# Optimization experiments

Hardware: AMD Instinct MI355X
Metric: run time of the kernel (lower is better)

## Reference

```python
import jax, jax.numpy as jnp
import numpy as np

B, TK, H = 32, 1024, 512
N = 2 * H          # hidden_dim * 2
AD = 512           # attention_dimension


def setup_inputs() -> dict:
    key = jax.random.key(0)
    ks = jax.random.split(key, 11)
    s = 0.02  # weight scale
    return {
        's_t_hat': jax.random.normal(ks[0], (B, N), jnp.float32),
        'encoder_outputs': jax.random.normal(ks[1], (B, TK, N), jnp.float32),
        'encoder_feature': jax.random.normal(ks[2], (B * TK, N), jnp.float32),
        'enc_padding_mask': jax.random.uniform(ks[3], (B, TK), jnp.float32),
        'coverage': jax.random.uniform(ks[4], (B, TK), jnp.float32),
        'r_i': jax.random.normal(ks[5], (B, TK, AD), jnp.float32),
        'W_s_w': jax.random.normal(ks[6], (N, N), jnp.float32) * s,
        'W_s_b': jax.random.normal(ks[7], (N,), jnp.float32) * s,
        'W_c_w': jax.random.normal(ks[8], (N, 1), jnp.float32) * s,
        'v_w': jax.random.normal(ks[9], (1, N), jnp.float32) * s,
        'W_r_w': jax.random.normal(ks[10], (N, AD), jnp.float32) * s,
    }


def reference(s_t_hat, encoder_outputs, encoder_feature, enc_padding_mask,
              coverage, r_i, W_s_w, W_s_b, W_c_w, v_w, W_r_w):
    b, t_k, n = encoder_outputs.shape
    # decoder feature: W_s(s_t_hat), broadcast over time
    dec_fea = s_t_hat @ W_s_w.T + W_s_b                       # [b, n]
    enc_feat = encoder_feature.reshape(b, t_k, n)             # [b, t_k, n]
    # coverage feature: W_c applied to scalar coverage per position
    cov_feat = coverage[..., None] * W_c_w[:, 0]              # [b, t_k, n]
    e = jnp.tanh(enc_feat + dec_fea[:, None, :] + cov_feat)   # [b, t_k, n]
    scores = jnp.einsum('btn,n->bt', e, v_w[0])               # [b, t_k]
    attn_ = jax.nn.softmax(scores, axis=1) * enc_padding_mask
    attn = attn_ / attn_.sum(1, keepdims=True)                # renormalized
    c_t = jnp.einsum('bt,btn->bn', attn, encoder_outputs)     # [b, n]
    coverage_new = coverage + attn                            # [b, t_k]
    # structural (LSA) branch
    Wrri = jnp.einsum('bta,na->btn', r_i, W_r_w)              # [b, t_k, n]
    e_s = jnp.tanh(Wrri + dec_fea[:, None, :])
    s2 = jnp.einsum('btn,n->bt', e_s, v_w[0])
    a_struct = (jax.nn.softmax(s2, axis=1) * enc_padding_mask)[:, None, :]  # [b,1,t_k]
    c_t_struct = jnp.einsum('bt,btn->bn', a_struct[:, 0], encoder_outputs)  # [b, n]
    return (c_t, attn, coverage_new, c_t_struct, a_struct)
```

## Files before the change

### kernel.cpp

```cpp
#include <hip/hip_runtime.h>
#include <hip/hip_bf16.h>

static constexpr int BB   = 32;
static constexpr int TKK  = 1024;
static constexpr int ND   = 1024;
static constexpr int ADIM = 512;

typedef __attribute__((ext_vector_type(8))) short bf16x8;
typedef __attribute__((ext_vector_type(4))) float f32x4;

__device__ __forceinline__ float fast_tanh(float x) {
  x = fminf(fmaxf(x, -15.f), 15.f);
  float e = __expf(2.f * x);
  return __fdividef(e - 1.f, e + 1.f);
}

__device__ __forceinline__ short f2bf(float x) {
  unsigned u = __float_as_uint(x);
  u += 0x7FFF + ((u >> 16) & 1);
  return (short)(u >> 16);
}

__device__ __forceinline__ void gload_lds16(const void* g, void* l) {
  __builtin_amdgcn_global_load_lds(
      (const __attribute__((address_space(1))) unsigned int*)g,
      (__attribute__((address_space(3))) unsigned int*)l, 16, 0, 0);
}

__global__ __launch_bounds__(256) void k_cvt2(const float* __restrict__ r_i,
    const float* __restrict__ Wr, short* __restrict__ rb, short* __restrict__ wb) {
  size_t bid = blockIdx.x;
  const float* src;
  short* dst;
  size_t i;
  if (bid < 8192) { src = r_i; dst = rb; i = bid * 256 + threadIdx.x; }
  else            { src = Wr;  dst = wb; i = (bid - 8192) * 256 + threadIdx.x; }
  float4 a = ((const float4*)src)[2 * i];
  float4 b = ((const float4*)src)[2 * i + 1];
  bf16x8 h;
  h[0] = f2bf(a.x); h[1] = f2bf(a.y); h[2] = f2bf(a.z); h[3] = f2bf(a.w);
  h[4] = f2bf(b.x); h[5] = f2bf(b.y); h[6] = f2bf(b.z); h[7] = f2bf(b.w);
  ((bf16x8*)dst)[i] = h;
}

__global__ __launch_bounds__(256) void k_decfea(const float* __restrict__ s_t_hat,
    const float* __restrict__ Wsw, const float* __restrict__ Wsb,
    float* __restrict__ dec) {
  int b  = blockIdx.x >> 3;
  int n0 = (blockIdx.x & 7) << 7;
  int w = threadIdx.x >> 6, lane = threadIdx.x & 63;
  const float4* s4 = (const float4*)(s_t_hat + (size_t)b * ND);
  float4 sv0 = s4[lane], sv1 = s4[lane + 64], sv2 = s4[lane + 128], sv3 = s4[lane + 192];
  for (int nn = 0; nn < 32; nn++) {
    int n = n0 + w * 32 + nn;
    const float4* w4 = (const float4*)(Wsw + (size_t)n * ND);
    float4 wa = w4[lane], wb = w4[lane + 64], wc = w4[lane + 128], wd = w4[lane + 192];
    float acc = sv0.x*wa.x + sv0.y*wa.y + sv0.z*wa.z + sv0.w*wa.w
              + sv1.x*wb.x + sv1.y*wb.y + sv1.z*wb.z + sv1.w*wb.w
              + sv2.x*wc.x + sv2.y*wc.y + sv2.z*wc.z + sv2.w*wc.w
              + sv3.x*wd.x + sv3.y*wd.y + sv3.z*wd.z + sv3.w*wd.w;
    #pragma unroll
    for (int off = 32; off; off >>= 1) acc += __shfl_down(acc, off);
    if (lane == 0) dec[b * ND + n] = acc + Wsb[n];
  }
}

__global__ __launch_bounds__(256) void k_scoresA(const float* __restrict__ ef,
    const float* __restrict__ dec, const float* __restrict__ Wc,
    const float* __restrict__ vw, const float* __restrict__ cov,
    float* __restrict__ scores) {
  __shared__ float sb[4];
  int bt = blockIdx.x;
  int b  = bt >> 10;
  int tid = threadIdx.x;
  float4 e = *(const float4*)(ef + (size_t)bt * ND + tid * 4);
  float4 d = *(const float4*)(dec + (size_t)b * ND + tid * 4);
  float4 w = *(const float4*)(Wc + tid * 4);
  float4 v = *(const float4*)(vw + tid * 4);
  float c = cov[bt];
  float s = v.x * fast_tanh(e.x + d.x + c * w.x)
          + v.y * fast_tanh(e.y + d.y + c * w.y)
          + v.z * fast_tanh(e.z + d.z + c * w.z)
          + v.w * fast_tanh(e.w + d.w + c * w.w);
  #pragma unroll
  for (int off = 32; off; off >>= 1) s += __shfl_down(s, off);
  if ((tid & 63) == 0) sb[tid >> 6] = s;
  __syncthreads();
  if (tid == 0) scores[bt] = sb[0] + sb[1] + sb[2] + sb[3];
}

__global__ __launch_bounds__(256) void k_softmaxA(const float* __restrict__ scores,
    const float* __restrict__ mask, const float* __restrict__ cov,
    float* __restrict__ attn, float* __restrict__ covnew) {
  __shared__ float sb[4];
  int b = blockIdx.x, tid = threadIdx.x;
  float4 s = *(const float4*)(scores + (size_t)b * TKK + tid * 4);
  float m = fmaxf(fmaxf(s.x, s.y), fmaxf(s.z, s.w));
  #pragma unroll
  for (int off = 32; off; off >>= 1) m = fmaxf(m, __shfl_down(m, off));
  if ((tid & 63) == 0) sb[tid >> 6] = m;
  __syncthreads();
  m = fmaxf(fmaxf(sb[0], sb[1]), fmaxf(sb[2], sb[3]));
  float4 mk = *(const float4*)(mask + (size_t)b * TKK + tid * 4);
  float4 e;
  e.x = __expf(s.x - m) * mk.x;
  e.y = __expf(s.y - m) * mk.y;
  e.z = __expf(s.z - m) * mk.z;
  e.w = __expf(s.w - m) * mk.w;
  float sum = e.x + e.y + e.z + e.w;
  #pragma unroll
  for (int off = 32; off; off >>= 1) sum += __shfl_down(sum, off);
  __syncthreads();
  if ((tid & 63) == 0) sb[tid >> 6] = sum;
  __syncthreads();
  float inv = __fdividef(1.f, sb[0] + sb[1] + sb[2] + sb[3]);
  float4 a = {e.x * inv, e.y * inv, e.z * inv, e.w * inv};
  *(float4*)(attn + (size_t)b * TKK + tid * 4) = a;
  float4 c = *(const float4*)(cov + (size_t)b * TKK + tid * 4);
  float4 cn = {c.x + a.x, c.y + a.y, c.z + a.z, c.w + a.w};
  *(float4*)(covnew + (size_t)b * TKK + tid * 4) = cn;
}

__global__ __launch_bounds__(512, 4) void k_gemmB4(const short* __restrict__ rb,
    const short* __restrict__ wb, const float* __restrict__ dec,
    const float* __restrict__ vw, float* __restrict__ part) {
  __shared__ __align__(16) short Bl[64 * ADIM];
  const int tid = threadIdx.x;
  const int lane = tid & 63, wv = tid >> 6;
  const int g = lane >> 4, cl = lane & 15;
  const int bid = blockIdx.x;
  const int swz = (bid & 7) * 256 + (bid >> 3);
  const int mchunk = swz >> 4, nchunk = swz & 15;
  const int b  = mchunk >> 2;
  const int t0 = (mchunk & 3) * 256;
  const int n0 = nchunk * 64;
  const short* Ag = rb + (size_t)(b * TKK + t0) * ADIM;
  const short* Bg = wb + (size_t)n0 * ADIM;

  #pragma unroll
  for (int it = 0; it < 8; ++it) {
    const int row = it * 8 + wv;
    gload_lds16(Bg + (size_t)row * ADIM + (size_t)((lane ^ (row & 7)) * 8),
                &Bl[row * ADIM]);
  }
  asm volatile("s_waitcnt vmcnt(0)" ::: "memory");
  __builtin_amdgcn_s_barrier();

  const int wrow = wv * 32;
  const short* a0 = Ag + (size_t)(wrow + cl) * ADIM + g * 8;
  const short* a1 = a0 + (size_t)16 * ADIM;

  f32x4 acc[2][4];
  #pragma unroll
  for (int m = 0; m < 2; ++m)
    #pragma unroll
    for (int n = 0; n < 4; ++n) acc[m][n] = (f32x4){0.f, 0.f, 0.f, 0.f};

  #pragma unroll
  for (int kc = 0; kc < 16; ++kc) {
    bf16x8 af0 = *(const bf16x8*)(a0 + kc * 32);
    bf16x8 af1 = *(const bf16x8*)(a1 + kc * 32);
    bf16x8 bfr[4];
    #pragma unroll
    for (int n = 0; n < 4; ++n)
      bfr[n] = *(const bf16x8*)&Bl[(n * 16 + cl) * ADIM
                                   + (((kc * 4 + g) ^ (cl & 7)) * 8)];
    #pragma unroll
    for (int n = 0; n < 4; ++n) {
      acc[0][n] = __builtin_amdgcn_mfma_f32_16x16x32_bf16(af0, bfr[n], acc[0][n], 0, 0, 0);
      acc[1][n] = __builtin_amdgcn_mfma_f32_16x16x32_bf16(af1, bfr[n], acc[1][n], 0, 0, 0);
    }
  }

  float vvv[4], ddd[4];
  #pragma unroll
  for (int n = 0; n < 4; ++n) {
    const int col = n0 + n * 16 + cl;
    vvv[n] = vw[col];
    ddd[n] = dec[b * ND + col];
  }
  #pragma unroll
  for (int mf = 0; mf < 2; ++mf) {
    #pragma unroll
    for (int r = 0; r < 4; ++r) {
      float s = 0.f;
      #pragma unroll
      for (int n = 0; n < 4; ++n)
        s += vvv[n] * fast_tanh(acc[mf][n][r] + ddd[n]);
      #pragma unroll
      for (int off = 1; off < 16; off <<= 1) s += __shfl_xor(s, off);
      if (cl == 0) {
        const int rowg = b * TKK + t0 + wrow + mf * 16 + g * 4 + r;
        part[(size_t)rowg * 16 + nchunk] = s;
      }
    }
  }
}

__global__ __launch_bounds__(256) void k_gemmB(const float* __restrict__ r_i,
    const float* __restrict__ Wr, const float* __restrict__ dec,
    const float* __restrict__ vw, float* __restrict__ part) {
  __shared__ short As[128 * 64];
  __shared__ short Bs[128 * 64];
  const int tid = threadIdx.x;
  const int lane = tid & 63, wv = tid >> 6;
  const int wm = wv >> 1, wn = wv & 1;
  const int g = lane >> 4, cl = lane & 15;
  const int mchunk = blockIdx.x, nchunk = blockIdx.y;
  const int b  = mchunk >> 3;
  const int t0 = (mchunk & 7) * 128;
  const int n0 = nchunk * 128;
  const float* Ag = r_i + (size_t)(b * TKK + t0) * ADIM;
  const float* Bg = Wr + (size_t)n0 * ADIM;
  const int srow = tid >> 3, skk = (tid & 7) * 8;

  f32x4 acc[4][4];
  #pragma unroll
  for (int m = 0; m < 4; ++m)
    #pragma unroll
    for (int n = 0; n < 4; ++n) acc[m][n] = (f32x4){0.f, 0.f, 0.f, 0.f};

  for (int kc = 0; kc < 8; ++kc) {
    const int k0 = kc * 64;
    __syncthreads();
    #pragma unroll
    for (int dit = 0; dit < 4; ++dit) {
      const int row = dit * 32 + srow;
      const float* sa = Ag + (size_t)row * ADIM + k0 + skk;
      float4 a0 = *(const float4*)sa, a1 = *(const float4*)(sa + 4);
      bf16x8 ha;
      ha[0]=f2bf(a0.x); ha[1]=f2bf(a0.y); ha[2]=f2bf(a0.z); ha[3]=f2bf(a0.w);
      ha[4]=f2bf(a1.x); ha[5]=f2bf(a1.y); ha[6]=f2bf(a1.z); ha[7]=f2bf(a1.w);
      *(bf16x8*)&As[row * 64 + skk] = ha;
      const float* sbp = Bg + (size_t)row * ADIM + k0 + skk;
      float4 b0 = *(const float4*)sbp, b1 = *(const float4*)(sbp + 4);
      bf16x8 hb;
      hb[0]=f2bf(b0.x); hb[1]=f2bf(b0.y); hb[2]=f2bf(b0.z); hb[3]=f2bf(b0.w);
      hb[4]=f2bf(b1.x); hb[5]=f2bf(b1.y); hb[6]=f2bf(b1.z); hb[7]=f2bf(b1.w);
      *(bf16x8*)&Bs[row * 64 + skk] = hb;
    }
    __syncthreads();
    #pragma unroll
    for (int kf = 0; kf < 2; ++kf) {
      bf16x8 af[4], bfr[4];
      #pragma unroll
      for (int m = 0; m < 4; ++m)
        af[m] = *(const bf16x8*)&As[(wm * 64 + m * 16 + cl) * 64 + kf * 32 + g * 8];
      #pragma unroll
      for (int n = 0; n < 4; ++n)
        bfr[n] = *(const bf16x8*)&Bs[(wn * 64 + n * 16 + cl) * 64 + kf * 32 + g * 8];
      #pragma unroll
      for (int m = 0; m < 4; ++m)
        #pragma unroll
        for (int n = 0; n < 4; ++n)
          acc[m][n] = __builtin_amdgcn_mfma_f32_16x16x32_bf16(af[m], bfr[n], acc[m][n], 0, 0, 0);
    }
  }
  float vvv[4], ddd[4];
  #pragma unroll
  for (int n = 0; n < 4; ++n) {
    const int col = n0 + wn * 64 + n * 16 + cl;
    vvv[n] = vw[col];
    ddd[n] = dec[b * ND + col];
  }
  #pragma unroll
  for (int m = 0; m < 4; ++m) {
    #pragma unroll
    for (int r = 0; r < 4; ++r) {
      float s = 0.f;
      #pragma unroll
      for (int n = 0; n < 4; ++n)
        s += vvv[n] * fast_tanh(acc[m][n][r] + ddd[n]);
      #pragma unroll
      for (int off = 1; off < 16; off <<= 1) s += __shfl_xor(s, off);
      if (cl == 0) {
        const int rowg = b * TKK + t0 + wm * 64 + m * 16 + g * 4 + r;
        part[(size_t)rowg * 16 + nchunk * 2 + wn] = s;
      }
    }
  }
}

__global__ __launch_bounds__(256) void k_softmaxB(const float* __restrict__ part,
    const float* __restrict__ mask, float* __restrict__ astruct) {
  __shared__ float sb[4];
  int b = blockIdx.x, tid = threadIdx.x;
  float sv[4];
  #pragma unroll
  for (int tt = 0; tt < 4; ++tt) {
    const float4* pp = (const float4*)(part + ((size_t)b * TKK + tid * 4 + tt) * 16);
    float4 q0 = pp[0], q1 = pp[1], q2 = pp[2], q3 = pp[3];
    sv[tt] = q0.x+q0.y+q0.z+q0.w + q1.x+q1.y+q1.z+q1.w
           + q2.x+q2.y+q2.z+q2.w + q3.x+q3.y+q3.z+q3.w;
  }
  float m = fmaxf(fmaxf(sv[0], sv[1]), fmaxf(sv[2], sv[3]));
  #pragma unroll
  for (int off = 32; off; off >>= 1) m = fmaxf(m, __shfl_down(m, off));
  if ((tid & 63) == 0) sb[tid >> 6] = m;
  __syncthreads();
  m = fmaxf(fmaxf(sb[0], sb[1]), fmaxf(sb[2], sb[3]));
  float e0 = __expf(sv[0] - m), e1 = __expf(sv[1] - m);
  float e2 = __expf(sv[2] - m), e3 = __expf(sv[3] - m);
  float sum = e0 + e1 + e2 + e3;
  #pragma unroll
  for (int off = 32; off; off >>= 1) sum += __shfl_down(sum, off);
  __syncthreads();
  if ((tid & 63) == 0) sb[tid >> 6] = sum;
  __syncthreads();
  float inv = __fdividef(1.f, sb[0] + sb[1] + sb[2] + sb[3]);
  float4 mk = *(const float4*)(mask + (size_t)b * TKK + tid * 4);
  float4 a = {e0 * mk.x * inv, e1 * mk.y * inv, e2 * mk.z * inv, e3 * mk.w * inv};
  *(float4*)(astruct + (size_t)b * TKK + tid * 4) = a;
}

__global__ __launch_bounds__(256) void k_ctx(const float* __restrict__ enc,
    const float* __restrict__ attn, const float* __restrict__ astr,
    float* __restrict__ partials) {
  int tc = blockIdx.x, b = blockIdx.y;
  int tid = threadIdx.x, lane = tid & 63;
  float a1v = attn[(size_t)b * TKK + tc * 64 + lane];
  float a2v = astr[(size_t)b * TKK + tc * 64 + lane];
  const float4* e4 = (const float4*)(enc + (size_t)(b * TKK + tc * 64) * ND);
  float4 ac = {0, 0, 0, 0}, as = {0, 0, 0, 0};
  #pragma unroll 4
  for (int m = 0; m < 64; m++) {
    float a1 = __shfl(a1v, m), a2 = __shfl(a2v, m);
    float4 ev = e4[(size_t)m * 256 + tid];
    ac.x += a1 * ev.x; ac.y += a1 * ev.y; ac.z += a1 * ev.z; ac.w += a1 * ev.w;
    as.x += a2 * ev.x; as.y += a2 * ev.y; as.z += a2 * ev.z; as.w += a2 * ev.w;
  }
  float* p = partials + (size_t)(b * 16 + tc) * 2 * ND;
  *(float4*)(p + tid * 4) = ac;
  *(float4*)(p + ND + tid * 4) = as;
}

__global__ __launch_bounds__(256) void k_reduce(const float* __restrict__ partials,
    float* __restrict__ ct, float* __restrict__ cts) {
  int b = blockIdx.x, tid = threadIdx.x;
  float4 sc = {0, 0, 0, 0}, ss = {0, 0, 0, 0};
  for (int tc = 0; tc < 16; tc++) {
    const float* p = partials + (size_t)(b * 16 + tc) * 2 * ND;
    float4 p1 = *(const float4*)(p + tid * 4);
    float4 p2 = *(const float4*)(p + ND + tid * 4);
    sc.x += p1.x; sc.y += p1.y; sc.z += p1.z; sc.w += p1.w;
    ss.x += p2.x; ss.y += p2.y; ss.z += p2.z; ss.w += p2.w;
  }
  *(float4*)(ct + (size_t)b * ND + tid * 4) = sc;
  *(float4*)(cts + (size_t)b * ND + tid * 4) = ss;
}

extern "C" void kernel_launch(void* const* d_in, const int* in_sizes, int n_in,
                              void* d_out, int out_size, void* d_ws, size_t ws_size,
                              hipStream_t stream) {
  const float* s_t_hat = (const float*)d_in[0];
  const float* enc_out  = (const float*)d_in[1];
  const float* enc_feat = (const float*)d_in[2];
  const float* mask     = (const float*)d_in[3];
  const float* cov      = (const float*)d_in[4];
  const float* r_i      = (const float*)d_in[5];
  const float* Wsw      = (const float*)d_in[6];
  const float* Wsb      = (const float*)d_in[7];
  const float* Wc       = (const float*)d_in[8];
  const float* vw       = (const float*)d_in[9];
  const float* Wr       = (const float*)d_in[10];

  float* out    = (float*)d_out;
  float* ct     = out;
  float* attn   = out + 32768;
  float* covnew = out + 65536;
  float* cts    = out + 98304;
  float* astr   = out + 131072;

  float* ws       = (float*)d_ws;
  float* dec      = ws;
  float* scores   = ws + 32768;
  float* s2part   = ws + 65536;
  float* partials = ws + 589824;
  short* rb       = (short*)(ws + 1638400);
  short* wb       = rb + 16777216;
  const size_t NEEDED = 1638400ull * 4 + 16777216ull * 2 + 524288ull * 2;

  k_decfea<<<256, 256, 0, stream>>>(s_t_hat, Wsw, Wsb, dec);
  k_scoresA<<<BB * TKK, 256, 0, stream>>>(enc_feat, dec, Wc, vw, cov, scores);
  k_softmaxA<<<BB, 256, 0, stream>>>(scores, mask, cov, attn, covnew);
  if (ws_size >= NEEDED) {
    k_cvt2<<<8448, 256, 0, stream>>>(r_i, Wr, rb, wb);
    k_gemmB4<<<2048, 512, 0, stream>>>(rb, wb, dec, vw, s2part);
  } else {
    k_gemmB<<<dim3(256, 8), 256, 0, stream>>>(r_i, Wr, dec, vw, s2part);
  }
  k_softmaxB<<<BB, 256, 0, stream>>>(s2part, mask, astr);
  k_ctx<<<dim3(16, BB), 256, 0, stream>>>(enc_out, attn, astr, partials);
  k_reduce<<<BB, 256, 0, stream>>>(partials, ct, cts);
}
```

Baseline: 190.4 us.

## Replace structural GEMM with 256x256-tile double-buffered pipelined MFMA kernel

Rewrites the structural-branch bf16 GEMM so each block computes a 256x256 output tile instead of 256x64. A and B are staged in 64-wide K slices through double-buffered LDS using async global-to-LDS loads, and the stages are interleaved with MFMA phases under fine-grained vmcnt waits and barriers. This cuts global reloads of the A operand (previously read 16 times, once per 64-column chunk) and hides load latency. The cost is 128KB of dynamic LDS per block, far fewer blocks (512), and heavy register use for accumulators.

```diff
diff --git a/kernel.cpp b/kernel.cpp
--- a/kernel.cpp
+++ b/kernel.cpp
@@ -121,77 +121,149 @@
   *(float4*)(covnew + (size_t)b * TKK + tid * 4) = cn;
 }
 
-__global__ __launch_bounds__(512, 4) void k_gemmB4(const short* __restrict__ rb,
+__global__ __launch_bounds__(512, 2) void k_gemm8(const short* __restrict__ rb,
     const short* __restrict__ wb, const float* __restrict__ dec,
     const float* __restrict__ vw, float* __restrict__ part) {
-  __shared__ __align__(16) short Bl[64 * ADIM];
+  extern __shared__ short lds[];
+  short* As = lds;
+  short* Bs = lds + 32768;
   const int tid = threadIdx.x;
   const int lane = tid & 63, wv = tid >> 6;
+  const int a2 = wv >> 2, b4 = wv & 3;
   const int g = lane >> 4, cl = lane & 15;
   const int bid = blockIdx.x;
-  const int swz = (bid & 7) * 256 + (bid >> 3);
-  const int mchunk = swz >> 4, nchunk = swz & 15;
+  const int swz = (bid & 7) * 64 + (bid >> 3);
+  const int mchunk = swz >> 2, nchunk = swz & 3;
   const int b  = mchunk >> 2;
   const int t0 = (mchunk & 3) * 256;
-  const int n0 = nchunk * 64;
+  const int n0 = nchunk * 256;
   const short* Ag = rb + (size_t)(b * TKK + t0) * ADIM;
   const short* Bg = wb + (size_t)n0 * ADIM;
-
-  #pragma unroll
-  for (int it = 0; it < 8; ++it) {
-    const int row = it * 8 + wv;
-    gload_lds16(Bg + (size_t)row * ADIM + (size_t)((lane ^ (row & 7)) * 8),
-                &Bl[row * ADIM]);
-  }
-  asm volatile("s_waitcnt vmcnt(0)" ::: "memory");
+  const int srow = lane >> 3;
+  const int sch  = ((lane & 7) ^ srow) * 8;
+
+  auto stageA = [&](int buf, int h, int tile) {
+    #pragma unroll
+    for (int p = 0; p < 2; ++p) {
+      const int rl = p * 64 + wv * 8;
+      gload_lds16(Ag + (size_t)(h * 128 + rl + srow) * ADIM + tile * 64 + sch,
+                  As + (buf * 2 + h) * 8192 + rl * 64);
+    }
+  };
+  auto stageB = [&](int buf, int h, int tile) {
+    #pragma unroll
+    for (int p = 0; p < 2; ++p) {
+      const int rl = p * 64 + wv * 8;
+      gload_lds16(Bg + (size_t)(h * 128 + rl + srow) * ADIM + tile * 64 + sch,
+                  Bs + (buf * 2 + h) * 8192 + rl * 64);
+    }
+  };
+
+  bf16x8 afr[4][2], bfr[2][2];
+  f32x4 acc[2][2][4][2];
+  #pragma unroll
+  for (int i = 0; i < 2; ++i)
+    #pragma unroll
+    for (int j = 0; j < 2; ++j)
+      #pragma unroll
+      for (int m = 0; m < 4; ++m)
+        #pragma unroll
+        for (int n = 0; n < 2; ++n) acc[i][j][m][n] = (f32x4){0.f, 0.f, 0.f, 0.f};
+
+  auto loadA = [&](int buf, int mq) {
+    #pragma unroll
+    for (int mf = 0; mf < 4; ++mf)
+      #pragma unroll
+      for (int kf = 0; kf < 2; ++kf) {
+        const int rl = a2 * 64 + mf * 16 + cl;
+        afr[mf][kf] = *(const bf16x8*)(As + (buf * 2 + mq) * 8192 + rl * 64
+                                       + (((kf * 4 + g) ^ (cl & 7)) * 8));
+      }
+  };
+  auto loadB = [&](int buf, int nq) {
+    #pragma unroll
+    for (int nf = 0; nf < 2; ++nf)
+      #pragma unroll
+      for (int kf = 0; kf < 2; ++kf) {
+        const int rl = b4 * 32 + nf * 16 + cl;
+        bfr[nf][kf] = *(const bf16x8*)(Bs + (buf * 2 + nq) * 8192 + rl * 64
+                                       + (((kf * 4 + g) ^ (cl & 7)) * 8));
+      }
+  };
+  auto domfma = [&](int mq, int nq) {
+    #pragma unroll
+    for (int kf = 0; kf < 2; ++kf)
+      #pragma unroll
+      for (int mf = 0; mf < 4; ++mf)
+        #pragma unroll
+        for (int nf = 0; nf < 2; ++nf)
+          acc[mq][nq][mf][nf] = __builtin_amdgcn_mfma_f32_16x16x32_bf16(
+              afr[mf][kf], bfr[nf][kf], acc[mq][nq][mf][nf], 0, 0, 0);
+  };
+
+#define PH(MQ, NQ, BUF, DOLOADA, STG, VM)                              \
+  do {                                                                 \
+    if (DOLOADA) loadA(BUF, MQ);                                       \
+    loadB(BUF, NQ);                                                    \
+    STG;                                                               \
+    if ((VM) == 4) asm volatile("s_waitcnt vmcnt(4)" ::: "memory");    \
+    if ((VM) == 0) asm volatile("s_waitcnt vmcnt(0)" ::: "memory");    \
+    __builtin_amdgcn_s_barrier();                                      \
+    asm volatile("s_waitcnt lgkmcnt(0)" ::: "memory");                 \
+    __builtin_amdgcn_sched_barrier(0);                                 \
+    __builtin_amdgcn_s_setprio(1);                                     \
+    domfma(MQ, NQ);                                                    \
+    __builtin_amdgcn_s_setprio(0);                                     \
+    __builtin_amdgcn_s_barrier();                                      \
+  } while (0)
+
+  stageA(0, 0, 0); stageB(0, 0, 0); stageA(0, 1, 0); stageB(0, 1, 0);
+  stageA(1, 0, 1); stageB(1, 0, 1);
+  asm volatile("s_waitcnt vmcnt(4)" ::: "memory");
   __builtin_amdgcn_s_barrier();
 
-  const int wrow = wv * 32;
-  const short* a0 = Ag + (size_t)(wrow + cl) * ADIM + g * 8;
-  const short* a1 = a0 + (size_t)16 * ADIM;
-
-  f32x4 acc[2][4];
-  #pragma unroll
-  for (int m = 0; m < 2; ++m)
-    #pragma unroll
-    for (int n = 0; n < 4; ++n) acc[m][n] = (f32x4){0.f, 0.f, 0.f, 0.f};
-
-  #pragma unroll
-  for (int kc = 0; kc < 16; ++kc) {
-    bf16x8 af0 = *(const bf16x8*)(a0 + kc * 32);
-    bf16x8 af1 = *(const bf16x8*)(a1 + kc * 32);
-    bf16x8 bfr[4];
-    #pragma unroll
-    for (int n = 0; n < 4; ++n)
-      bfr[n] = *(const bf16x8*)&Bl[(n * 16 + cl) * ADIM
-                                   + (((kc * 4 + g) ^ (cl & 7)) * 8)];
-    #pragma unroll
-    for (int n = 0; n < 4; ++n) {
-      acc[0][n] = __builtin_amdgcn_mfma_f32_16x16x32_bf16(af0, bfr[n], acc[0][n], 0, 0, 0);
-      acc[1][n] = __builtin_amdgcn_mfma_f32_16x16x32_bf16(af1, bfr[n], acc[1][n], 0, 0, 0);
-    }
-  }
-
-  float vvv[4], ddd[4];
-  #pragma unroll
-  for (int n = 0; n < 4; ++n) {
-    const int col = n0 + n * 16 + cl;
-    vvv[n] = vw[col];
-    ddd[n] = dec[b * ND + col];
-  }
-  #pragma unroll
-  for (int mf = 0; mf < 2; ++mf) {
-    #pragma unroll
-    for (int r = 0; r < 4; ++r) {
-      float s = 0.f;
-      #pragma unroll
-      for (int n = 0; n < 4; ++n)
-        s += vvv[n] * fast_tanh(acc[mf][n][r] + ddd[n]);
-      #pragma unroll
-      for (int off = 1; off < 16; off <<= 1) s += __shfl_xor(s, off);
-      if (cl == 0) {
-        const int rowg = b * TKK + t0 + wrow + mf * 16 + g * 4 + r;
-        part[(size_t)rowg * 16 + nchunk] = s;
+  #pragma unroll
+  for (int it = 0; it < 4; ++it) {
+    const int T = 2 * it;
+    const bool more = (it < 3);
+    PH(0, 0, 0, true,  { stageA(1, 1, T + 1); }, -1);
+    PH(0, 1, 0, false, { stageB(1, 1, T + 1); }, -1);
+    PH(1, 0, 0, true,  { if (more) stageA(0, 0, T + 2); }, -1);
+    PH(1, 1, 0, false, { if (more) stageB(0, 0, T + 2); }, (more ? 4 : 0));
+    PH(0, 0, 1, true,  { if (more) stageA(0, 1, T + 2); }, -1);
+    PH(0, 1, 1, false, { if (more) stageB(0, 1, T + 2); }, -1);
+    PH(1, 0, 1, true,  { if (more) stageA(1, 0, T + 3); }, -1);
+    PH(1, 1, 1, false, { if (more) stageB(1, 0, T + 3); }, (more ? 4 : 0));
+  }
+#undef PH
+
+  float vvv[2][2], ddd[2][2];
+  #pragma unroll
+  for (int nq = 0; nq < 2; ++nq)
+    #pragma unroll
+    for (int nf = 0; nf < 2; ++nf) {
+      const int col = n0 + nq * 128 + b4 * 32 + nf * 16 + cl;
+      vvv[nq][nf] = vw[col];
+      ddd[nq][nf] = dec[b * ND + col];
+    }
+  #pragma unroll
+  for (int mq = 0; mq < 2; ++mq) {
+    #pragma unroll
+    for (int mf = 0; mf < 4; ++mf) {
+      #pragma unroll
+      for (int r = 0; r < 4; ++r) {
+        float s = 0.f;
+        #pragma unroll
+        for (int nq = 0; nq < 2; ++nq)
+          #pragma unroll
+          for (int nf = 0; nf < 2; ++nf)
+            s += vvv[nq][nf] * fast_tanh(acc[mq][nq][mf][nf][r] + ddd[nq][nf]);
+        #pragma unroll
+        for (int off = 1; off < 16; off <<= 1) s += __shfl_xor(s, off);
+        if (cl == 0) {
+          const int rowg = b * TKK + t0 + mq * 128 + a2 * 64 + mf * 16 + g * 4 + r;
+          part[(size_t)rowg * 16 + nchunk * 4 + b4] = s;
+        }
       }
     }
   }
@@ -385,7 +457,7 @@
   k_softmaxA<<<BB, 256, 0, stream>>>(scores, mask, cov, attn, covnew);
   if (ws_size >= NEEDED) {
     k_cvt2<<<8448, 256, 0, stream>>>(r_i, Wr, rb, wb);
-    k_gemmB4<<<2048, 512, 0, stream>>>(rb, wb, dec, vw, s2part);
+    k_gemm8<<<512, 512, 131072, stream>>>(rb, wb, dec, vw, s2part);
   } else {
     k_gemmB<<<dim3(256, 8), 256, 0, stream>>>(r_i, Wr, dec, vw, s2part);
   }
```

New measurement: 174.8 us. 8.2% less time.
